# Kernel optimization log

Hardware: AMD Instinct MI355X
Metric: run time of the kernel (lower is better)

## Reference

```python
import jax, jax.numpy as jnp
import numpy as np

DIM = 128
EDGE_COUNT = 128
N_NODES = 128
GRAPH_COUNT = 8
VOCAB = 100000
VEC_DIM = 300


def setup_inputs():
    key = jax.random.key(0)
    ks = jax.random.split(key, 8)
    rng = np.random.default_rng(0)
    data = jnp.asarray(rng.integers(0, VOCAB, size=N_NODES), dtype=jnp.int32)
    types = jnp.zeros((N_NODES,), dtype=jnp.int32)  # single data_type
    edges = jnp.asarray(rng.integers(0, EDGE_COUNT, size=N_NODES), dtype=jnp.int32)
    # parent-offset trees: node i's parent is a node > i, last node is the single root (offset 0)
    g = np.zeros((GRAPH_COUNT, N_NODES), dtype=np.int32)
    for j in range(GRAPH_COUNT):
        for i in range(N_NODES - 1):
            p = int(rng.integers(i + 1, N_NODES))
            g[j, i] = p - i
    graphs = jnp.asarray(g)
    inv_sqrt_d = 1.0 / np.sqrt(DIM)
    inv_sqrt_v = 1.0 / np.sqrt(VEC_DIM)
    return {
        "data": data, "types": types, "graphs": graphs, "edges": edges, "pos": 37,
        "data_vecs": jax.random.normal(ks[0], (VOCAB, VEC_DIM), jnp.float32),
        "data_weights": jax.random.normal(ks[1], (VEC_DIM, DIM), jnp.float32) * inv_sqrt_v,
        "data_biases": jax.random.normal(ks[2], (DIM,), jnp.float32) * 0.1,
        "edge_weights": jax.random.normal(ks[3], (EDGE_COUNT, DIM, DIM), jnp.float32) * inv_sqrt_d,
        "edge_biases": jax.random.normal(ks[4], (EDGE_COUNT, DIM), jnp.float32) * 0.1,
        "score_embedding_weights": jax.random.normal(ks[5], (DIM, 1), jnp.float32) * inv_sqrt_d,
        "score_data_weights": jax.random.normal(ks[6], (DIM, 1), jnp.float32) * inv_sqrt_d,
        "score_bias": jax.random.normal(ks[7], (1, 1), jnp.float32),
    }


def _tree_structure(parents_row):
    # Faithful reproduction of calc_embedding's structure handling (numpy on int constants).
    parents = np.asarray(parents_row).copy()
    n = len(parents)
    roots = [i for i in range(n) if parents[i] == 0]
    for i in range(len(roots) - 1):
        parents[roots[i]] = roots[i + 1]
    root = roots[-1]
    parents[root] = -n
    children = {}
    for i in range(n):
        pp = i + int(parents[i])
        children.setdefault(pp, []).append(i)
    order = []  # DFS preorder from root; reversed gives children-before-parent
    stack = [root]
    while stack:
        node = stack.pop()
        order.append(node)
        stack.extend(children.get(node, []))
    return root, children, order


def _forward(data, types, graphs, edges, pos,
             data_vecs, data_weights, data_biases,
             edge_weights, edge_biases,
             score_embedding_weights, score_data_weights, score_bias):
    data_np = np.asarray(data)
    graphs_np = np.asarray(graphs)
    edges_np = np.asarray(edges).copy()
    E, D, _ = edge_weights.shape
    # data embedding + data score for the queried position
    d_emb = data_vecs[data_np[pos]] @ data_weights + data_biases          # (D,)
    d_score = score_bias[0, 0] + d_emb @ score_data_weights[:, 0]         # scalar
    edges_np[pos] = -1  # unknown edge at pos -> branch over all edge types
    # base embeddings for all nodes at once: (N, D)
    base = data_vecs[data_np] @ data_weights + data_biases

    def transform(child_emb, eid):
        # child_emb: (E, D). eid < 0 -> per-edge-type weights (baddbmm over all E edges)
        if eid < 0:
            return jnp.einsum('ed,edk->ek', child_emb, edge_weights) + edge_biases
        return child_emb @ edge_weights[eid] + edge_biases[eid]

    scores = []
    for j in range(graphs_np.shape[0]):
        root, children, order = _tree_structure(graphs_np[j])
        emb = {}
        for n in reversed(order):  # children before parents
            e = jnp.broadcast_to(base[n], (E, D))
            ch = children.get(n, [])
            for c in ch:
                e = e + transform(emb.pop(c), int(edges_np[c]))
            if ch:
                e = jax.nn.relu(e)  # clamp(min=0) only for internal nodes
            emb[n] = e
        res = transform(emb[root], int(edges_np[root]))  # add_child_embedding(zeros, root_emb, edges[root])
        scores.append(d_score + res @ score_embedding_weights[:, 0])  # (E,)
    return jnp.stack(scores)  # (GRAPH_COUNT, EDGE_COUNT)


def reference(data, types, graphs, edges, pos, data_vecs, data_weights, data_biases,
              edge_weights, edge_biases, score_embedding_weights, score_data_weights, score_bias):
    return _forward(data, types, graphs, edges, pos, data_vecs, data_weights, data_biases,
                    edge_weights, edge_biases, score_embedding_weights, score_data_weights, score_bias)
```

## Files before the change

kernel.cpp:

```cpp
#include <hip/hip_runtime.h>
#include <stdint.h>


#define NND 128
#define DD  128
#define GG  8
#define VD  300
#define EDGEN 128
#define CH2 16

typedef unsigned int u32;

#define F_POS  (1<<16)
#define F_PATH (1<<17)

__global__ void __launch_bounds__(128) k_base(
        const int* __restrict__ data, const int* __restrict__ posArr,
        const float* __restrict__ vecs, const float* __restrict__ dw,
        const float* __restrict__ db,   const float* __restrict__ sdw,
        const float* __restrict__ sb,
        float* __restrict__ base, float* __restrict__ dscore)
{
    __shared__ __align__(16) float row[VD];
    __shared__ float red[DD];
    int n = blockIdx.x, t = threadIdx.x;
    int id = data[n];
    const float4* vp = (const float4*)(vecs + (size_t)id * VD);
    for (int i = t; i < VD/4; i += 128) ((float4*)row)[i] = vp[i];
    __syncthreads();
    float a0 = db[t], a1 = 0.f, a2 = 0.f, a3 = 0.f;
    for (int d = 0; d < VD; d += 4){
        a0 = fmaf(row[d+0], dw[(d+0)*DD + t], a0);
        a1 = fmaf(row[d+1], dw[(d+1)*DD + t], a1);
        a2 = fmaf(row[d+2], dw[(d+2)*DD + t], a2);
        a3 = fmaf(row[d+3], dw[(d+3)*DD + t], a3);
    }
    float acc = (a0 + a1) + (a2 + a3);
    base[n*DD + t] = acc;
    if (n == posArr[0]){
        red[t] = acc * sdw[t];
        __syncthreads();
        for (int o = 64; o > 0; o >>= 1){ if (t < o) red[t] += red[t+o]; __syncthreads(); }
        if (t == 0) dscore[0] = sb[0] + red[0];
    }
}

__global__ void __launch_bounds__(1024, 1) k_tree(
        const int* __restrict__ graphs, const int* __restrict__ edges,
        const int* __restrict__ posArr, const float* __restrict__ EW,
        const float* __restrict__ EB,   const float* __restrict__ base,
        float* __restrict__ vposG, float* __restrict__ uG, int* __restrict__ meta)
{
    __shared__ __align__(16) float contrib[NND-1][DD];
    __shared__ int par_s[NND], eid_s[NND], flg_s[NND];
    __shared__ int ccnt[NND], cstart[NND], cidx[NND];
    __shared__ int dep[NND], anc[NND], lcnt[NND], lstart[NND], order[NND];
    __shared__ int maxD_s;

    int g = blockIdx.x, t = threadIdx.x;

    if (t < NND){
        par_s[t] = (t < NND-1) ? (t + graphs[g*NND + t]) : (NND-1);
        eid_s[t] = edges[t];
        flg_s[t] = 0;
        ccnt[t]  = 0;
        lcnt[t]  = 0;
    }
    if (t == 0) maxD_s = 0;
    __syncthreads();

    int mySlot = 0;
    if (t < NND-1){
        int p = par_s[t];
        atomicAdd(&ccnt[p], 1);
        for (int c = 0; c < t; ++c) mySlot += (par_s[c] == p);
    }
    if (t < NND){
        dep[t] = (t < NND-1) ? 1 : 0;
        anc[t] = par_s[t];
    }
    if (t == 0){
        int p = posArr[0];
        flg_s[p] |= F_POS;
        int c = par_s[p], s = 0;
        for (;;){
            flg_s[c] |= F_PATH | (s << 24);
            meta[g*(NND+1) + 1 + s] = c;
            ++s;
            if (c == NND-1) break;
            c = par_s[c];
        }
        meta[g*(NND+1)] = s;
    }
    __syncthreads();

    if (t < NND){
        int s = 0;
        for (int p = 0; p < t; ++p) s += ccnt[p];
        cstart[t] = s;
    }
    __syncthreads();
    if (t < NND-1) cidx[cstart[par_s[t]] + mySlot] = t;

    for (int k = 0; k < 7; ++k){
        int d2 = 0, a2 = 0;
        if (t < NND){ d2 = dep[t] + dep[anc[t]]; a2 = anc[anc[t]]; }
        __syncthreads();
        if (t < NND){ dep[t] = d2; anc[t] = a2; }
        __syncthreads();
    }
    if (t < NND) atomicMax(&maxD_s, dep[t]);
    if (t < NND) atomicAdd(&lcnt[dep[t]], 1);
    __syncthreads();

    if (t < NND){
        int s = 0;
        for (int d2 = 0; d2 < t; ++d2) s += lcnt[d2];
        lstart[t] = s;
    }
    __syncthreads();
    if (t < NND){
        int d2 = dep[t], s = 0;
        for (int c = 0; c < t; ++c) s += (dep[c] == d2);
        order[lstart[d2] + s] = t;
    }
    __syncthreads();

    int w = t >> 6, l = t & 63;
    int c0 = 2*l;
    int li = l & 31, hl = l >> 5;
    int c4 = 4*li, dbase = 64*hl;
    int maxD = maxD_s;

    for (int d = maxD; d >= 0; --d){
        int lo = lstart[d], cnt = lcnt[d];
        for (int q = w; q < cnt; q += 16){
            int n = order[lo + q];
            float2 bse = *(const float2*)&base[n*DD + c0];
            float e0 = bse.x, e1 = bse.y;
            int cs = cstart[n], cc = ccnt[n];
            for (int j = 0; j < cc; ++j){
                int c = cidx[cs + j];
                if (!(flg_s[c] & (F_POS | F_PATH))){
                    float2 cv = *(const float2*)&contrib[c][c0];
                    e0 += cv.x; e1 += cv.y;
                }
            }
            int f = flg_s[n];
            if (f & F_POS){
                if (cc){ e0 = fmaxf(e0, 0.f); e1 = fmaxf(e1, 0.f); }
                *(float2*)&vposG[g*DD + c0] = make_float2(e0, e1);
            } else if (f & F_PATH){
                int slot = ((u32)f) >> 24;
                *(float2*)&uG[((size_t)g*NND + slot)*DD + c0] = make_float2(e0, e1);
            } else {
                if (cc){ e0 = fmaxf(e0, 0.f); e1 = fmaxf(e1, 0.f); }
                *(float2*)&contrib[n][c0] = make_float2(e0, e1);
                asm volatile("s_waitcnt lgkmcnt(0)" ::: "memory");
                int e = eid_s[n];
                const float* Wp = EW + (size_t)e*(DD*DD) + (size_t)dbase*DD + c4;
                const float* xr = &contrib[n][dbase];
                float4 A[8], B[8];
                float s0=0.f, s1=0.f, s2=0.f, s3=0.f;
                #define LW(buf, gi) { _Pragma("unroll") \
                    for (int j2 = 0; j2 < 8; ++j2) \
                        buf[j2] = *(const float4*)&Wp[(size_t)((gi)*8 + j2)*DD]; }
                #define CP(buf, gi) { _Pragma("unroll") \
                    for (int j2 = 0; j2 < 8; ++j2){ \
                        float x = xr[(gi)*8 + j2]; \
                        s0 = fmaf(x, buf[j2].x, s0); s1 = fmaf(x, buf[j2].y, s1); \
                        s2 = fmaf(x, buf[j2].z, s2); s3 = fmaf(x, buf[j2].w, s3); } }
                LW(A,0); LW(B,1);
                CP(A,0); LW(A,2);
                CP(B,1); LW(B,3);
                CP(A,2); LW(A,4);
                CP(B,3); LW(B,5);
                CP(A,4); LW(A,6);
                CP(B,5); LW(B,7);
                CP(A,6);
                CP(B,7);
                #undef LW
                #undef CP
                s0 += __shfl_xor(s0, 32);
                s1 += __shfl_xor(s1, 32);
                s2 += __shfl_xor(s2, 32);
                s3 += __shfl_xor(s3, 32);
                if (hl == 0){
                    float4 bb = *(const float4*)&EB[(size_t)e*DD + c4];
                    *(float4*)&contrib[n][c4] =
                        make_float4(s0 + bb.x, s1 + bb.y, s2 + bb.z, s3 + bb.w);
                }
            }
        }
        __syncthreads();
    }
}

__global__ void __launch_bounds__(256, 1) k_step0(
        const float* __restrict__ EW, const float* __restrict__ EB,
        const float* __restrict__ vposG, const float* __restrict__ uG,
        float* __restrict__ V0)
{
    __shared__ __align__(16) float vpos_s[GG][DD];
    int e = blockIdx.x, t = threadIdx.x, l = t & 63, w = t >> 6;
    {
        int idx = t;
        ((float4*)vpos_s)[idx] = ((const float4*)vposG)[idx];
    }
    __syncthreads();
    int k4 = w*8 + (l & 7);
    int d0 = (l >> 3) * 16;
    bool owner = ((l >> 3) == 0);
    const float* Wp = EW + (size_t)e*(DD*DD) + (size_t)d0*DD + 4*k4;
    float4 wr[16];
    #pragma unroll
    for (int d = 0; d < 16; ++d) wr[d] = *(const float4*)&Wp[d*DD];
    float4 bb = *(const float4*)&EB[(size_t)e*DD + 4*k4];
    for (int g = 0; g < GG; ++g){
        float s0=0.f, s1=0.f, s2=0.f, s3=0.f;
        #pragma unroll
        for (int d = 0; d < 16; ++d){
            float x = vpos_s[g][d0 + d];
            s0 = fmaf(x, wr[d].x, s0);
            s1 = fmaf(x, wr[d].y, s1);
            s2 = fmaf(x, wr[d].z, s2);
            s3 = fmaf(x, wr[d].w, s3);
        }
        #pragma unroll
        for (int m = 8; m <= 32; m <<= 1){
            s0 += __shfl_xor(s0, m); s1 += __shfl_xor(s1, m);
            s2 += __shfl_xor(s2, m); s3 += __shfl_xor(s3, m);
        }
        if (owner){
            float4 u0 = *(const float4*)&uG[(size_t)g*NND*DD + 4*k4];
            float4 r;
            r.x = fmaxf(u0.x + s0 + bb.x, 0.f);
            r.y = fmaxf(u0.y + s1 + bb.y, 0.f);
            r.z = fmaxf(u0.z + s2 + bb.z, 0.f);
            r.w = fmaxf(u0.w + s3 + bb.w, 0.f);
            *(float4*)&V0[((size_t)g*EDGEN + e)*DD + 4*k4] = r;
        }
    }
}

__global__ void __launch_bounds__(256, 1) k_steps(
        const int* __restrict__ edges,
        const float* __restrict__ EW, const float* __restrict__ EB,
        const float* __restrict__ SEW,
        const float* __restrict__ uG, const float* __restrict__ V0,
        const int* __restrict__ meta, const float* __restrict__ dscore,
        float* __restrict__ outp)
{
    __shared__ __align__(16) float Vbuf[2][CH2][DD];
    __shared__ float red[CH2][4];
    int g = blockIdx.x >> 3, chunk = blockIdx.x & 7;
    int t = threadIdx.x, l = t & 63, w = t >> 6;
    int k4 = w*8 + (l & 7);
    int d0 = (l >> 3) * 16;
    bool owner = ((l >> 3) == 0);
    int eBase = chunk * CH2;
    int L = meta[g*(NND+1)];

    for (int idx = t; idx < CH2*DD/4; idx += 256)
        ((float4*)&Vbuf[0][0][0])[idx] =
            ((const float4*)&V0[((size_t)g*EDGEN + eBase)*DD])[idx];
    __syncthreads();

    int cur = 0;
    for (int s = 1; s < L; ++s){
        int pn = meta[g*(NND+1) + s];
        int ej = edges[pn];
        const float* Wp = EW + (size_t)ej*(DD*DD) + (size_t)d0*DD + 4*k4;
        float4 wr[16];
        #pragma unroll
        for (int d = 0; d < 16; ++d) wr[d] = *(const float4*)&Wp[d*DD];
        float4 us = *(const float4*)&uG[((size_t)g*NND + s)*DD + 4*k4];
        float4 bb = *(const float4*)&EB[(size_t)ej*DD + 4*k4];
        #pragma unroll 4
        for (int p = 0; p < CH2; ++p){
            float ev[16];
            #pragma unroll
            for (int j = 0; j < 4; ++j){
                float4 x = *(const float4*)&Vbuf[cur][p][d0 + 4*j];
                ev[4*j+0]=x.x; ev[4*j+1]=x.y; ev[4*j+2]=x.z; ev[4*j+3]=x.w;
            }
            float s0=0.f, s1=0.f, s2=0.f, s3=0.f;
            #pragma unroll
            for (int d = 0; d < 16; ++d){
                s0 = fmaf(ev[d], wr[d].x, s0);
                s1 = fmaf(ev[d], wr[d].y, s1);
                s2 = fmaf(ev[d], wr[d].z, s2);
                s3 = fmaf(ev[d], wr[d].w, s3);
            }
            #pragma unroll
            for (int m = 8; m <= 32; m <<= 1){
                s0 += __shfl_xor(s0, m); s1 += __shfl_xor(s1, m);
                s2 += __shfl_xor(s2, m); s3 += __shfl_xor(s3, m);
            }
            if (owner){
                float4 r;
                r.x = fmaxf(us.x + s0 + bb.x, 0.f);
                r.y = fmaxf(us.y + s1 + bb.y, 0.f);
                r.z = fmaxf(us.z + s2 + bb.z, 0.f);
                r.w = fmaxf(us.w + s3 + bb.w, 0.f);
                *(float4*)&Vbuf[cur^1][p][4*k4] = r;
            }
        }
        __syncthreads();
        cur ^= 1;
    }

    {
        int rn = meta[g*(NND+1) + L];
        int er = edges[rn];
        const float* Wp = EW + (size_t)er*(DD*DD) + (size_t)d0*DD + 4*k4;
        float4 wr[16];
        #pragma unroll
        for (int d = 0; d < 16; ++d) wr[d] = *(const float4*)&Wp[d*DD];
        float4 bb = *(const float4*)&EB[(size_t)er*DD + 4*k4];
        float4 sw = *(const float4*)&SEW[4*k4];
        #pragma unroll 4
        for (int p = 0; p < CH2; ++p){
            float ev[16];
            #pragma unroll
            for (int j = 0; j < 4; ++j){
                float4 x = *(const float4*)&Vbuf[cur][p][d0 + 4*j];
                ev[4*j+0]=x.x; ev[4*j+1]=x.y; ev[4*j+2]=x.z; ev[4*j+3]=x.w;
            }
            float s0=0.f, s1=0.f, s2=0.f, s3=0.f;
            #pragma unroll
            for (int d = 0; d < 16; ++d){
                s0 = fmaf(ev[d], wr[d].x, s0);
                s1 = fmaf(ev[d], wr[d].y, s1);
                s2 = fmaf(ev[d], wr[d].z, s2);
                s3 = fmaf(ev[d], wr[d].w, s3);
            }
            #pragma unroll
            for (int m = 8; m <= 32; m <<= 1){
                s0 += __shfl_xor(s0, m); s1 += __shfl_xor(s1, m);
                s2 += __shfl_xor(s2, m); s3 += __shfl_xor(s3, m);
            }
            if (owner){
                float part = (s0 + bb.x) * sw.x + (s1 + bb.y) * sw.y
                           + (s2 + bb.z) * sw.z + (s3 + bb.w) * sw.w;
                part += __shfl_xor(part, 1);
                part += __shfl_xor(part, 2);
                part += __shfl_xor(part, 4);
                if (l == 0) red[p][w] = part;
            }
        }
        __syncthreads();
        if (t < CH2)
            outp[g*DD + eBase + t] = dscore[0] + red[t][0] + red[t][1] + red[t][2] + red[t][3];
    }
}

extern "C" void kernel_launch(void* const* d_in, const int* in_sizes, int n_in,
                              void* d_out, int out_size, void* d_ws, size_t ws_size,
                              hipStream_t stream)
{
    const int*   data   = (const int*)d_in[0];
    const int*   graphs = (const int*)d_in[2];
    const int*   edges  = (const int*)d_in[3];
    const int*   posArr = (const int*)d_in[4];
    const float* vecs   = (const float*)d_in[5];
    const float* dw     = (const float*)d_in[6];
    const float* db     = (const float*)d_in[7];
    const float* ew     = (const float*)d_in[8];
    const float* eb     = (const float*)d_in[9];
    const float* sew    = (const float*)d_in[10];
    const float* sdw    = (const float*)d_in[11];
    const float* sb     = (const float*)d_in[12];

    char* ws = (char*)d_ws;
    float* base   = (float*)(ws);
    float* vposG  = (float*)(ws + 65536);
    float* uG     = (float*)(ws + 65536 + 4096);
    float* dscore = (float*)(ws + 593920);
    int*   meta   = (int*)  (ws + 594176);
    float* V0     = (float*)(ws + 598528);

    float* outp = (float*)d_out;

    k_base <<<NND, 128, 0, stream>>>(data, posArr, vecs, dw, db, sdw, sb, base, dscore);
    k_tree <<<GG, 1024, 0, stream>>>(graphs, edges, posArr, ew, eb, base, vposG, uG, meta);
    k_step0<<<EDGEN, 256, 0, stream>>>(ew, eb, vposG, uG, V0);
    k_steps<<<GG*(EDGEN/CH2), 256, 0, stream>>>(edges, ew, eb, sew, uG, V0, meta, dscore, outp);
}
```

Measured before the change: 345.8 us.

## Fuse base embedding and step0 into tree and chain kernels, pair tree GEMVs

The base-embedding kernel is folded into the tree kernel, so each tree block recomputes all node base rows in shared-memory tiles. The first chain step is folded into the chain kernel, so V0 is computed in place instead of going through a global round trip and a separate launch. Inside the tree level loop each wave now handles two nodes at once and interleaves their weight loads, to get more memory-level parallelism on a latency-bound dependency chain. In exchange, the base GEMV work is repeated in every graph block and the step0 weights are re-read per graph chunk.

```diff
diff --git a/kernel.cpp b/kernel.cpp
--- a/kernel.cpp
+++ b/kernel.cpp
@@ -14,41 +14,14 @@
 #define F_POS  (1<<16)
 #define F_PATH (1<<17)
 
-__global__ void __launch_bounds__(128) k_base(
-        const int* __restrict__ data, const int* __restrict__ posArr,
+__global__ void __launch_bounds__(1024, 1) k_tree2(
+        const int* __restrict__ data,   const int* __restrict__ graphs,
+        const int* __restrict__ edges,  const int* __restrict__ posArr,
         const float* __restrict__ vecs, const float* __restrict__ dw,
         const float* __restrict__ db,   const float* __restrict__ sdw,
         const float* __restrict__ sb,
-        float* __restrict__ base, float* __restrict__ dscore)
-{
-    __shared__ __align__(16) float row[VD];
-    __shared__ float red[DD];
-    int n = blockIdx.x, t = threadIdx.x;
-    int id = data[n];
-    const float4* vp = (const float4*)(vecs + (size_t)id * VD);
-    for (int i = t; i < VD/4; i += 128) ((float4*)row)[i] = vp[i];
-    __syncthreads();
-    float a0 = db[t], a1 = 0.f, a2 = 0.f, a3 = 0.f;
-    for (int d = 0; d < VD; d += 4){
-        a0 = fmaf(row[d+0], dw[(d+0)*DD + t], a0);
-        a1 = fmaf(row[d+1], dw[(d+1)*DD + t], a1);
-        a2 = fmaf(row[d+2], dw[(d+2)*DD + t], a2);
-        a3 = fmaf(row[d+3], dw[(d+3)*DD + t], a3);
-    }
-    float acc = (a0 + a1) + (a2 + a3);
-    base[n*DD + t] = acc;
-    if (n == posArr[0]){
-        red[t] = acc * sdw[t];
-        __syncthreads();
-        for (int o = 64; o > 0; o >>= 1){ if (t < o) red[t] += red[t+o]; __syncthreads(); }
-        if (t == 0) dscore[0] = sb[0] + red[0];
-    }
-}
-
-__global__ void __launch_bounds__(1024, 1) k_tree(
-        const int* __restrict__ graphs, const int* __restrict__ edges,
-        const int* __restrict__ posArr, const float* __restrict__ EW,
-        const float* __restrict__ EB,   const float* __restrict__ base,
+        const float* __restrict__ EW,   const float* __restrict__ EB,
+        float* __restrict__ base, float* __restrict__ dscore,
         float* __restrict__ vposG, float* __restrict__ uG, int* __restrict__ meta)
 {
     __shared__ __align__(16) float contrib[NND-1][DD];
@@ -58,6 +31,38 @@
     __shared__ int maxD_s;
 
     int g = blockIdx.x, t = threadIdx.x;
+
+    {
+        float* rowbuf = &contrib[0][0];
+        for (int tile = 0; tile < 16; ++tile){
+            for (int i = t; i < 8*75; i += 1024){
+                int r = i / 75, el = i - r*75;
+                int nn = tile*8 + r;
+                ((float4*)&rowbuf[r*304])[el] =
+                    ((const float4*)&vecs[(size_t)data[nn]*VD])[el];
+            }
+            __syncthreads();
+            int r = t >> 7, c = t & 127;
+            int nn = tile*8 + r;
+            const float* rb = &rowbuf[r*304];
+            float a0 = db[c], a1 = 0.f, a2 = 0.f, a3 = 0.f;
+            for (int d = 0; d < VD; d += 4){
+                a0 = fmaf(rb[d+0], dw[(d+0)*DD + c], a0);
+                a1 = fmaf(rb[d+1], dw[(d+1)*DD + c], a1);
+                a2 = fmaf(rb[d+2], dw[(d+2)*DD + c], a2);
+                a3 = fmaf(rb[d+3], dw[(d+3)*DD + c], a3);
+            }
+            base[nn*DD + c] = (a0 + a1) + (a2 + a3);
+            __syncthreads();
+        }
+        int p = posArr[0];
+        float* red = rowbuf;
+        if (t < DD) red[t] = base[p*DD + t] * sdw[t];
+        __syncthreads();
+        for (int o = 64; o > 0; o >>= 1){ if (t < o) red[t] += red[t+o]; __syncthreads(); }
+        if (t == 0) dscore[0] = sb[0] + red[0];
+        __syncthreads();
+    }
 
     if (t < NND){
         par_s[t] = (t < NND-1) ? (t + graphs[g*NND + t]) : (NND-1);
@@ -132,122 +137,147 @@
     int c4 = 4*li, dbase = 64*hl;
     int maxD = maxD_s;
 
+    auto prep = [&](int n)->bool{
+        float2 bse = *(const float2*)&base[n*DD + c0];
+        float e0 = bse.x, e1 = bse.y;
+        int cs = cstart[n], cc = ccnt[n];
+        for (int j = 0; j < cc; ++j){
+            int c = cidx[cs + j];
+            if (!(flg_s[c] & (F_POS | F_PATH))){
+                float2 cv = *(const float2*)&contrib[c][c0];
+                e0 += cv.x; e1 += cv.y;
+            }
+        }
+        int f = flg_s[n];
+        if (f & F_POS){
+            if (cc){ e0 = fmaxf(e0, 0.f); e1 = fmaxf(e1, 0.f); }
+            *(float2*)&vposG[g*DD + c0] = make_float2(e0, e1);
+            return false;
+        }
+        if (f & F_PATH){
+            int slot = ((u32)f) >> 24;
+            *(float2*)&uG[((size_t)g*NND + slot)*DD + c0] = make_float2(e0, e1);
+            return false;
+        }
+        if (cc){ e0 = fmaxf(e0, 0.f); e1 = fmaxf(e1, 0.f); }
+        *(float2*)&contrib[n][c0] = make_float2(e0, e1);
+        return true;
+    };
+
+    auto gemv1 = [&](int n){
+        int e = eid_s[n];
+        const float* Wp = EW + (size_t)e*(DD*DD) + (size_t)dbase*DD + c4;
+        const float* xr = &contrib[n][dbase];
+        float4 A[8], B[8];
+        float s0=0.f, s1=0.f, s2=0.f, s3=0.f;
+        #define LW(buf, gi) { _Pragma("unroll") \
+            for (int j2 = 0; j2 < 8; ++j2) \
+                buf[j2] = *(const float4*)&Wp[(size_t)((gi)*8 + j2)*DD]; }
+        #define CP(buf, gi) { _Pragma("unroll") \
+            for (int j2 = 0; j2 < 8; ++j2){ \
+                float x = xr[(gi)*8 + j2]; \
+                s0 = fmaf(x, buf[j2].x, s0); s1 = fmaf(x, buf[j2].y, s1); \
+                s2 = fmaf(x, buf[j2].z, s2); s3 = fmaf(x, buf[j2].w, s3); } }
+        LW(A,0); LW(B,1);
+        CP(A,0); LW(A,2);
+        CP(B,1); LW(B,3);
+        CP(A,2); LW(A,4);
+        CP(B,3); LW(B,5);
+        CP(A,4); LW(A,6);
+        CP(B,5); LW(B,7);
+        CP(A,6);
+        CP(B,7);
+        #undef LW
+        #undef CP
+        s0 += __shfl_xor(s0, 32); s1 += __shfl_xor(s1, 32);
+        s2 += __shfl_xor(s2, 32); s3 += __shfl_xor(s3, 32);
+        if (hl == 0){
+            float4 bb = *(const float4*)&EB[(size_t)e*DD + c4];
+            *(float4*)&contrib[n][c4] =
+                make_float4(s0 + bb.x, s1 + bb.y, s2 + bb.z, s3 + bb.w);
+        }
+    };
+
+    auto gemv2 = [&](int n1, int n2){
+        int ea = eid_s[n1], eb = eid_s[n2];
+        const float* W1 = EW + (size_t)ea*(DD*DD) + (size_t)dbase*DD + c4;
+        const float* W2 = EW + (size_t)eb*(DD*DD) + (size_t)dbase*DD + c4;
+        const float* x1 = &contrib[n1][dbase];
+        const float* x2 = &contrib[n2][dbase];
+        float4 A[8], B[8];
+        float a0=0.f,a1=0.f,a2=0.f,a3=0.f, b0=0.f,b1=0.f,b2=0.f,b3=0.f;
+        #define LW1(gi) { _Pragma("unroll") \
+            for (int j2 = 0; j2 < 8; ++j2) \
+                A[j2] = *(const float4*)&W1[(size_t)((gi)*8 + j2)*DD]; }
+        #define LW2(gi) { _Pragma("unroll") \
+            for (int j2 = 0; j2 < 8; ++j2) \
+                B[j2] = *(const float4*)&W2[(size_t)((gi)*8 + j2)*DD]; }
+        #define CP1(gi) { _Pragma("unroll") \
+            for (int j2 = 0; j2 < 8; ++j2){ \
+                float x = x1[(gi)*8 + j2]; \
+                a0 = fmaf(x, A[j2].x, a0); a1 = fmaf(x, A[j2].y, a1); \
+                a2 = fmaf(x, A[j2].z, a2); a3 = fmaf(x, A[j2].w, a3); } }
+        #define CP2(gi) { _Pragma("unroll") \
+            for (int j2 = 0; j2 < 8; ++j2){ \
+                float x = x2[(gi)*8 + j2]; \
+                b0 = fmaf(x, B[j2].x, b0); b1 = fmaf(x, B[j2].y, b1); \
+                b2 = fmaf(x, B[j2].z, b2); b3 = fmaf(x, B[j2].w, b3); } }
+        LW1(0); LW2(0);
+        CP1(0); LW1(1);
+        CP2(0); LW2(1);
+        CP1(1); LW1(2);
+        CP2(1); LW2(2);
+        CP1(2); LW1(3);
+        CP2(2); LW2(3);
+        CP1(3); LW1(4);
+        CP2(3); LW2(4);
+        CP1(4); LW1(5);
+        CP2(4); LW2(5);
+        CP1(5); LW1(6);
+        CP2(5); LW2(6);
+        CP1(6); LW1(7);
+        CP2(6); LW2(7);
+        CP1(7);
+        CP2(7);
+        #undef LW1
+        #undef LW2
+        #undef CP1
+        #undef CP2
+        a0 += __shfl_xor(a0, 32); a1 += __shfl_xor(a1, 32);
+        a2 += __shfl_xor(a2, 32); a3 += __shfl_xor(a3, 32);
+        b0 += __shfl_xor(b0, 32); b1 += __shfl_xor(b1, 32);
+        b2 += __shfl_xor(b2, 32); b3 += __shfl_xor(b3, 32);
+        if (hl == 0){
+            float4 ba = *(const float4*)&EB[(size_t)ea*DD + c4];
+            float4 bb = *(const float4*)&EB[(size_t)eb*DD + c4];
+            *(float4*)&contrib[n1][c4] =
+                make_float4(a0 + ba.x, a1 + ba.y, a2 + ba.z, a3 + ba.w);
+            *(float4*)&contrib[n2][c4] =
+                make_float4(b0 + bb.x, b1 + bb.y, b2 + bb.z, b3 + bb.w);
+        }
+    };
+
     for (int d = maxD; d >= 0; --d){
         int lo = lstart[d], cnt = lcnt[d];
-        for (int q = w; q < cnt; q += 16){
-            int n = order[lo + q];
-            float2 bse = *(const float2*)&base[n*DD + c0];
-            float e0 = bse.x, e1 = bse.y;
-            int cs = cstart[n], cc = ccnt[n];
-            for (int j = 0; j < cc; ++j){
-                int c = cidx[cs + j];
-                if (!(flg_s[c] & (F_POS | F_PATH))){
-                    float2 cv = *(const float2*)&contrib[c][c0];
-                    e0 += cv.x; e1 += cv.y;
-                }
-            }
-            int f = flg_s[n];
-            if (f & F_POS){
-                if (cc){ e0 = fmaxf(e0, 0.f); e1 = fmaxf(e1, 0.f); }
-                *(float2*)&vposG[g*DD + c0] = make_float2(e0, e1);
-            } else if (f & F_PATH){
-                int slot = ((u32)f) >> 24;
-                *(float2*)&uG[((size_t)g*NND + slot)*DD + c0] = make_float2(e0, e1);
-            } else {
-                if (cc){ e0 = fmaxf(e0, 0.f); e1 = fmaxf(e1, 0.f); }
-                *(float2*)&contrib[n][c0] = make_float2(e0, e1);
-                asm volatile("s_waitcnt lgkmcnt(0)" ::: "memory");
-                int e = eid_s[n];
-                const float* Wp = EW + (size_t)e*(DD*DD) + (size_t)dbase*DD + c4;
-                const float* xr = &contrib[n][dbase];
-                float4 A[8], B[8];
-                float s0=0.f, s1=0.f, s2=0.f, s3=0.f;
-                #define LW(buf, gi) { _Pragma("unroll") \
-                    for (int j2 = 0; j2 < 8; ++j2) \
-                        buf[j2] = *(const float4*)&Wp[(size_t)((gi)*8 + j2)*DD]; }
-                #define CP(buf, gi) { _Pragma("unroll") \
-                    for (int j2 = 0; j2 < 8; ++j2){ \
-                        float x = xr[(gi)*8 + j2]; \
-                        s0 = fmaf(x, buf[j2].x, s0); s1 = fmaf(x, buf[j2].y, s1); \
-                        s2 = fmaf(x, buf[j2].z, s2); s3 = fmaf(x, buf[j2].w, s3); } }
-                LW(A,0); LW(B,1);
-                CP(A,0); LW(A,2);
-                CP(B,1); LW(B,3);
-                CP(A,2); LW(A,4);
-                CP(B,3); LW(B,5);
-                CP(A,4); LW(A,6);
-                CP(B,5); LW(B,7);
-                CP(A,6);
-                CP(B,7);
-                #undef LW
-                #undef CP
-                s0 += __shfl_xor(s0, 32);
-                s1 += __shfl_xor(s1, 32);
-                s2 += __shfl_xor(s2, 32);
-                s3 += __shfl_xor(s3, 32);
-                if (hl == 0){
-                    float4 bb = *(const float4*)&EB[(size_t)e*DD + c4];
-                    *(float4*)&contrib[n][c4] =
-                        make_float4(s0 + bb.x, s1 + bb.y, s2 + bb.z, s3 + bb.w);
-                }
-            }
+        for (int q = w; q < cnt; q += 32){
+            int n1 = order[lo + q];
+            int n2 = (q + 16 < cnt) ? order[lo + q + 16] : -1;
+            bool p1 = prep(n1);
+            bool p2 = (n2 >= 0) ? prep(n2) : false;
+            asm volatile("s_waitcnt lgkmcnt(0)" ::: "memory");
+            if (p1 && p2)      gemv2(n1, n2);
+            else { if (p1) gemv1(n1);
+                   if (p2) gemv1(n2); }
         }
         __syncthreads();
     }
 }
 
-__global__ void __launch_bounds__(256, 1) k_step0(
-        const float* __restrict__ EW, const float* __restrict__ EB,
-        const float* __restrict__ vposG, const float* __restrict__ uG,
-        float* __restrict__ V0)
-{
-    __shared__ __align__(16) float vpos_s[GG][DD];
-    int e = blockIdx.x, t = threadIdx.x, l = t & 63, w = t >> 6;
-    {
-        int idx = t;
-        ((float4*)vpos_s)[idx] = ((const float4*)vposG)[idx];
-    }
-    __syncthreads();
-    int k4 = w*8 + (l & 7);
-    int d0 = (l >> 3) * 16;
-    bool owner = ((l >> 3) == 0);
-    const float* Wp = EW + (size_t)e*(DD*DD) + (size_t)d0*DD + 4*k4;
-    float4 wr[16];
-    #pragma unroll
-    for (int d = 0; d < 16; ++d) wr[d] = *(const float4*)&Wp[d*DD];
-    float4 bb = *(const float4*)&EB[(size_t)e*DD + 4*k4];
-    for (int g = 0; g < GG; ++g){
-        float s0=0.f, s1=0.f, s2=0.f, s3=0.f;
-        #pragma unroll
-        for (int d = 0; d < 16; ++d){
-            float x = vpos_s[g][d0 + d];
-            s0 = fmaf(x, wr[d].x, s0);
-            s1 = fmaf(x, wr[d].y, s1);
-            s2 = fmaf(x, wr[d].z, s2);
-            s3 = fmaf(x, wr[d].w, s3);
-        }
-        #pragma unroll
-        for (int m = 8; m <= 32; m <<= 1){
-            s0 += __shfl_xor(s0, m); s1 += __shfl_xor(s1, m);
-            s2 += __shfl_xor(s2, m); s3 += __shfl_xor(s3, m);
-        }
-        if (owner){
-            float4 u0 = *(const float4*)&uG[(size_t)g*NND*DD + 4*k4];
-            float4 r;
-            r.x = fmaxf(u0.x + s0 + bb.x, 0.f);
-            r.y = fmaxf(u0.y + s1 + bb.y, 0.f);
-            r.z = fmaxf(u0.z + s2 + bb.z, 0.f);
-            r.w = fmaxf(u0.w + s3 + bb.w, 0.f);
-            *(float4*)&V0[((size_t)g*EDGEN + e)*DD + 4*k4] = r;
-        }
-    }
-}
-
-__global__ void __launch_bounds__(256, 1) k_steps(
+__global__ void __launch_bounds__(256, 1) k_chain2(
         const int* __restrict__ edges,
         const float* __restrict__ EW, const float* __restrict__ EB,
         const float* __restrict__ SEW,
-        const float* __restrict__ uG, const float* __restrict__ V0,
+        const float* __restrict__ vposG, const float* __restrict__ uG,
         const int* __restrict__ meta, const float* __restrict__ dscore,
         float* __restrict__ outp)
 {
@@ -261,9 +291,42 @@
     int eBase = chunk * CH2;
     int L = meta[g*(NND+1)];
 
-    for (int idx = t; idx < CH2*DD/4; idx += 256)
-        ((float4*)&Vbuf[0][0][0])[idx] =
-            ((const float4*)&V0[((size_t)g*EDGEN + eBase)*DD])[idx];
+    float vpf[16];
+    #pragma unroll
+    for (int j = 0; j < 4; ++j){
+        float4 x = *(const float4*)&vposG[g*DD + d0 + 4*j];
+        vpf[4*j+0]=x.x; vpf[4*j+1]=x.y; vpf[4*j+2]=x.z; vpf[4*j+3]=x.w;
+    }
+    float4 u0 = *(const float4*)&uG[(size_t)g*NND*DD + 4*k4];
+
+    #pragma unroll 2
+    for (int p = 0; p < CH2; ++p){
+        int e = eBase + p;
+        const float* Wp = EW + (size_t)e*(DD*DD) + (size_t)d0*DD + 4*k4;
+        float s0=0.f, s1=0.f, s2=0.f, s3=0.f;
+        #pragma unroll
+        for (int d = 0; d < 16; ++d){
+            float4 wv = *(const float4*)&Wp[d*DD];
+            s0 = fmaf(vpf[d], wv.x, s0);
+            s1 = fmaf(vpf[d], wv.y, s1);
+            s2 = fmaf(vpf[d], wv.z, s2);
+            s3 = fmaf(vpf[d], wv.w, s3);
+        }
+        #pragma unroll
+        for (int m = 8; m <= 32; m <<= 1){
+            s0 += __shfl_xor(s0, m); s1 += __shfl_xor(s1, m);
+            s2 += __shfl_xor(s2, m); s3 += __shfl_xor(s3, m);
+        }
+        if (owner){
+            float4 bb = *(const float4*)&EB[(size_t)e*DD + 4*k4];
+            float4 r;
+            r.x = fmaxf(u0.x + s0 + bb.x, 0.f);
+            r.y = fmaxf(u0.y + s1 + bb.y, 0.f);
+            r.z = fmaxf(u0.z + s2 + bb.z, 0.f);
+            r.w = fmaxf(u0.w + s3 + bb.w, 0.f);
+            *(float4*)&Vbuf[0][p][4*k4] = r;
+        }
+    }
     __syncthreads();
 
     int cur = 0;
@@ -375,15 +438,14 @@
     char* ws = (char*)d_ws;
     float* base   = (float*)(ws);
     float* vposG  = (float*)(ws + 65536);
-    float* uG     = (float*)(ws + 65536 + 4096);
+    float* uG     = (float*)(ws + 69632);
     float* dscore = (float*)(ws + 593920);
     int*   meta   = (int*)  (ws + 594176);
-    float* V0     = (float*)(ws + 598528);
 
     float* outp = (float*)d_out;
 
-    k_base <<<NND, 128, 0, stream>>>(data, posArr, vecs, dw, db, sdw, sb, base, dscore);
-    k_tree <<<GG, 1024, 0, stream>>>(graphs, edges, posArr, ew, eb, base, vposG, uG, meta);
-    k_step0<<<EDGEN, 256, 0, stream>>>(ew, eb, vposG, uG, V0);
-    k_steps<<<GG*(EDGEN/CH2), 256, 0, stream>>>(edges, ew, eb, sew, uG, V0, meta, dscore, outp);
+    k_tree2 <<<GG, 1024, 0, stream>>>(data, graphs, edges, posArr, vecs, dw, db,
+                                      sdw, sb, ew, eb, base, dscore, vposG, uG, meta);
+    k_chain2<<<GG*(EDGEN/CH2), 256, 0, stream>>>(edges, ew, eb, sew, vposG, uG,
+                                                 meta, dscore, outp);
 }
```

Measured after the change: 526.4 us. +52.2%, slower.

## Replace level-synchronous tree traversal with dataflow work queue in k_tree

Applied to the files above, without the earlier changes.

Drops the pointer-jumping depth computation and the per-level __syncthreads loop in the tree kernel. Each wavefront now pulls ready nodes from a shared-memory queue, and a node's parent is enqueued once its child counter reaches zero. This removes block-wide barriers and load imbalance across depth levels, so independent subtrees can proceed concurrently. The cost is spin-waiting on queue slots and atomics, plus reliance on volatile LDS polling and waitcnt for correct ordering.

```diff
diff --git a/kernel.cpp b/kernel.cpp
--- a/kernel.cpp
+++ b/kernel.cpp
@@ -54,8 +54,9 @@
     __shared__ __align__(16) float contrib[NND-1][DD];
     __shared__ int par_s[NND], eid_s[NND], flg_s[NND];
     __shared__ int ccnt[NND], cstart[NND], cidx[NND];
-    __shared__ int dep[NND], anc[NND], lcnt[NND], lstart[NND], order[NND];
-    __shared__ int maxD_s;
+    __shared__ int kcnt[NND];
+    __shared__ int queue[NND];
+    __shared__ int qhead, qtail;
 
     int g = blockIdx.x, t = threadIdx.x;
 
@@ -64,9 +65,9 @@
         eid_s[t] = edges[t];
         flg_s[t] = 0;
         ccnt[t]  = 0;
-        lcnt[t]  = 0;
-    }
-    if (t == 0) maxD_s = 0;
+        queue[t] = -1;
+    }
+    if (t == 0){ qhead = 0; qtail = 0; }
     __syncthreads();
 
     int mySlot = 0;
@@ -74,10 +75,6 @@
         int p = par_s[t];
         atomicAdd(&ccnt[p], 1);
         for (int c = 0; c < t; ++c) mySlot += (par_s[c] == p);
-    }
-    if (t < NND){
-        dep[t] = (t < NND-1) ? 1 : 0;
-        anc[t] = par_s[t];
     }
     if (t == 0){
         int p = posArr[0];
@@ -98,101 +95,102 @@
         int s = 0;
         for (int p = 0; p < t; ++p) s += ccnt[p];
         cstart[t] = s;
+        kcnt[t] = ccnt[t];
     }
     __syncthreads();
     if (t < NND-1) cidx[cstart[par_s[t]] + mySlot] = t;
-
-    for (int k = 0; k < 7; ++k){
-        int d2 = 0, a2 = 0;
-        if (t < NND){ d2 = dep[t] + dep[anc[t]]; a2 = anc[anc[t]]; }
-        __syncthreads();
-        if (t < NND){ dep[t] = d2; anc[t] = a2; }
-        __syncthreads();
-    }
-    if (t < NND) atomicMax(&maxD_s, dep[t]);
-    if (t < NND) atomicAdd(&lcnt[dep[t]], 1);
-    __syncthreads();
-
-    if (t < NND){
-        int s = 0;
-        for (int d2 = 0; d2 < t; ++d2) s += lcnt[d2];
-        lstart[t] = s;
-    }
-    __syncthreads();
-    if (t < NND){
-        int d2 = dep[t], s = 0;
-        for (int c = 0; c < t; ++c) s += (dep[c] == d2);
-        order[lstart[d2] + s] = t;
-    }
-    __syncthreads();
-
-    int w = t >> 6, l = t & 63;
+    if (t < NND && ccnt[t] == 0){
+        int slot = atomicAdd(&qtail, 1);
+        queue[slot] = t;
+    }
+    __syncthreads();
+
+    int l = t & 63;
     int c0 = 2*l;
     int li = l & 31, hl = l >> 5;
     int c4 = 4*li, dbase = 64*hl;
-    int maxD = maxD_s;
-
-    for (int d = maxD; d >= 0; --d){
-        int lo = lstart[d], cnt = lcnt[d];
-        for (int q = w; q < cnt; q += 16){
-            int n = order[lo + q];
-            float2 bse = *(const float2*)&base[n*DD + c0];
-            float e0 = bse.x, e1 = bse.y;
-            int cs = cstart[n], cc = ccnt[n];
-            for (int j = 0; j < cc; ++j){
-                int c = cidx[cs + j];
-                if (!(flg_s[c] & (F_POS | F_PATH))){
-                    float2 cv = *(const float2*)&contrib[c][c0];
-                    e0 += cv.x; e1 += cv.y;
-                }
-            }
-            int f = flg_s[n];
-            if (f & F_POS){
-                if (cc){ e0 = fmaxf(e0, 0.f); e1 = fmaxf(e1, 0.f); }
-                *(float2*)&vposG[g*DD + c0] = make_float2(e0, e1);
-            } else if (f & F_PATH){
-                int slot = ((u32)f) >> 24;
-                *(float2*)&uG[((size_t)g*NND + slot)*DD + c0] = make_float2(e0, e1);
-            } else {
-                if (cc){ e0 = fmaxf(e0, 0.f); e1 = fmaxf(e1, 0.f); }
-                *(float2*)&contrib[n][c0] = make_float2(e0, e1);
-                asm volatile("s_waitcnt lgkmcnt(0)" ::: "memory");
-                int e = eid_s[n];
-                const float* Wp = EW + (size_t)e*(DD*DD) + (size_t)dbase*DD + c4;
-                const float* xr = &contrib[n][dbase];
-                float4 A[8], B[8];
-                float s0=0.f, s1=0.f, s2=0.f, s3=0.f;
-                #define LW(buf, gi) { _Pragma("unroll") \
-                    for (int j2 = 0; j2 < 8; ++j2) \
-                        buf[j2] = *(const float4*)&Wp[(size_t)((gi)*8 + j2)*DD]; }
-                #define CP(buf, gi) { _Pragma("unroll") \
-                    for (int j2 = 0; j2 < 8; ++j2){ \
-                        float x = xr[(gi)*8 + j2]; \
-                        s0 = fmaf(x, buf[j2].x, s0); s1 = fmaf(x, buf[j2].y, s1); \
-                        s2 = fmaf(x, buf[j2].z, s2); s3 = fmaf(x, buf[j2].w, s3); } }
-                LW(A,0); LW(B,1);
-                CP(A,0); LW(A,2);
-                CP(B,1); LW(B,3);
-                CP(A,2); LW(A,4);
-                CP(B,3); LW(B,5);
-                CP(A,4); LW(A,6);
-                CP(B,5); LW(B,7);
-                CP(A,6);
-                CP(B,7);
-                #undef LW
-                #undef CP
-                s0 += __shfl_xor(s0, 32);
-                s1 += __shfl_xor(s1, 32);
-                s2 += __shfl_xor(s2, 32);
-                s3 += __shfl_xor(s3, 32);
-                if (hl == 0){
-                    float4 bb = *(const float4*)&EB[(size_t)e*DD + c4];
-                    *(float4*)&contrib[n][c4] =
-                        make_float4(s0 + bb.x, s1 + bb.y, s2 + bb.z, s3 + bb.w);
-                }
-            }
-        }
-        __syncthreads();
+
+    auto prep = [&](int n)->bool{
+        float2 bse = *(const float2*)&base[n*DD + c0];
+        float e0 = bse.x, e1 = bse.y;
+        int cs = cstart[n], cc = ccnt[n];
+        for (int j = 0; j < cc; ++j){
+            int c = cidx[cs + j];
+            if (!(flg_s[c] & (F_POS | F_PATH))){
+                float2 cv = *(const float2*)&contrib[c][c0];
+                e0 += cv.x; e1 += cv.y;
+            }
+        }
+        int f = flg_s[n];
+        if (f & F_POS){
+            if (cc){ e0 = fmaxf(e0, 0.f); e1 = fmaxf(e1, 0.f); }
+            *(float2*)&vposG[g*DD + c0] = make_float2(e0, e1);
+            return false;
+        }
+        if (f & F_PATH){
+            int slot = ((u32)f) >> 24;
+            *(float2*)&uG[((size_t)g*NND + slot)*DD + c0] = make_float2(e0, e1);
+            return false;
+        }
+        if (cc){ e0 = fmaxf(e0, 0.f); e1 = fmaxf(e1, 0.f); }
+        *(float2*)&contrib[n][c0] = make_float2(e0, e1);
+        return true;
+    };
+
+    auto gemv1 = [&](int n){
+        int e = eid_s[n];
+        const float* Wp = EW + (size_t)e*(DD*DD) + (size_t)dbase*DD + c4;
+        const float* xr = &contrib[n][dbase];
+        float4 A[8], B[8];
+        float s0=0.f, s1=0.f, s2=0.f, s3=0.f;
+        #define LW(buf, gi) { _Pragma("unroll") \
+            for (int j2 = 0; j2 < 8; ++j2) \
+                buf[j2] = *(const float4*)&Wp[(size_t)((gi)*8 + j2)*DD]; }
+        #define CP(buf, gi) { _Pragma("unroll") \
+            for (int j2 = 0; j2 < 8; ++j2){ \
+                float x = xr[(gi)*8 + j2]; \
+                s0 = fmaf(x, buf[j2].x, s0); s1 = fmaf(x, buf[j2].y, s1); \
+                s2 = fmaf(x, buf[j2].z, s2); s3 = fmaf(x, buf[j2].w, s3); } }
+        LW(A,0); LW(B,1);
+        CP(A,0); LW(A,2);
+        CP(B,1); LW(B,3);
+        CP(A,2); LW(A,4);
+        CP(B,3); LW(B,5);
+        CP(A,4); LW(A,6);
+        CP(B,5); LW(B,7);
+        CP(A,6);
+        CP(B,7);
+        #undef LW
+        #undef CP
+        s0 += __shfl_xor(s0, 32); s1 += __shfl_xor(s1, 32);
+        s2 += __shfl_xor(s2, 32); s3 += __shfl_xor(s3, 32);
+        if (hl == 0){
+            float4 bb = *(const float4*)&EB[(size_t)e*DD + c4];
+            *(float4*)&contrib[n][c4] =
+                make_float4(s0 + bb.x, s1 + bb.y, s2 + bb.z, s3 + bb.w);
+        }
+    };
+
+    for (;;){
+        int idx = 0;
+        if (l == 0) idx = atomicAdd(&qhead, 1);
+        idx = __shfl(idx, 0);
+        if (idx >= NND) break;
+        volatile int* qp = (volatile int*)&queue[idx];
+        int n;
+        while ((n = *qp) < 0) ;
+        bool doG = prep(n);
+        asm volatile("s_waitcnt lgkmcnt(0)" ::: "memory");
+        if (doG) gemv1(n);
+        asm volatile("s_waitcnt lgkmcnt(0)" ::: "memory");
+        if (l == 0 && n != NND-1){
+            int p = par_s[n];
+            int old = atomicSub(&kcnt[p], 1);
+            if (old == 1){
+                int slot = atomicAdd(&qtail, 1);
+                queue[slot] = p;
+            }
+        }
     }
 }
 
@@ -375,7 +373,7 @@
     char* ws = (char*)d_ws;
     float* base   = (float*)(ws);
     float* vposG  = (float*)(ws + 65536);
-    float* uG     = (float*)(ws + 65536 + 4096);
+    float* uG     = (float*)(ws + 69632);
     float* dscore = (float*)(ws + 593920);
     int*   meta   = (int*)  (ws + 594176);
     float* V0     = (float*)(ws + 598528);
@@ -385,5 +383,6 @@
     k_base <<<NND, 128, 0, stream>>>(data, posArr, vecs, dw, db, sdw, sb, base, dscore);
     k_tree <<<GG, 1024, 0, stream>>>(graphs, edges, posArr, ew, eb, base, vposG, uG, meta);
     k_step0<<<EDGEN, 256, 0, stream>>>(ew, eb, vposG, uG, V0);
-    k_steps<<<GG*(EDGEN/CH2), 256, 0, stream>>>(edges, ew, eb, sew, uG, V0, meta, dscore, outp);
-}
+    k_steps<<<GG*(EDGEN/CH2), 256, 0, stream>>>(edges, ew, eb, sew, uG, V0,
+                                                meta, dscore, outp);
+}
```

New measurement: 341.2 us. Within noise of the previous version (-1.3%).

## Split each tree across eight cooperating blocks with global per-level barriers

Applied to the files above, without the earlier changes.

The tree kernel now runs eight blocks per graph instead of one. Nodes within each depth level are interleaved across those blocks, and child contributions are exchanged through a global buffer that aliases V0 rather than living in shared memory. Blocks synchronise after each level with an atomic counter and spin-wait, and the counters are zeroed in k_base. The aim is to spread the edge-weight matvec streaming over more compute units. In exchange it adds global-memory traffic and per-level barrier latency, and it relies on all 64 blocks being resident at once.

```diff
diff --git a/kernel.cpp b/kernel.cpp
--- a/kernel.cpp
+++ b/kernel.cpp
@@ -8,22 +8,26 @@
 #define VD  300
 #define EDGEN 128
 #define CH2 16
+#define KSP 8
 
 typedef unsigned int u32;
 
 #define F_POS  (1<<16)
 #define F_PATH (1<<17)
+#define SKIPF  (F_POS|F_PATH)
 
 __global__ void __launch_bounds__(128) k_base(
         const int* __restrict__ data, const int* __restrict__ posArr,
         const float* __restrict__ vecs, const float* __restrict__ dw,
         const float* __restrict__ db,   const float* __restrict__ sdw,
         const float* __restrict__ sb,
-        float* __restrict__ base, float* __restrict__ dscore)
+        float* __restrict__ base, float* __restrict__ dscore,
+        int* __restrict__ flagsG)
 {
     __shared__ __align__(16) float row[VD];
     __shared__ float red[DD];
     int n = blockIdx.x, t = threadIdx.x;
+    if (n < GG) flagsG[n*NND + t] = 0;
     int id = data[n];
     const float4* vp = (const float4*)(vecs + (size_t)id * VD);
     for (int i = t; i < VD/4; i += 128) ((float4*)row)[i] = vp[i];
@@ -45,19 +49,20 @@
     }
 }
 
-__global__ void __launch_bounds__(1024, 1) k_tree(
+__global__ void __launch_bounds__(1024, 1) k_treeX(
         const int* __restrict__ graphs, const int* __restrict__ edges,
         const int* __restrict__ posArr, const float* __restrict__ EW,
         const float* __restrict__ EB,   const float* __restrict__ base,
-        float* __restrict__ vposG, float* __restrict__ uG, int* __restrict__ meta)
+        float* __restrict__ vposG, float* __restrict__ uG, int* __restrict__ meta,
+        float* __restrict__ contribX, int* __restrict__ flagsG)
 {
-    __shared__ __align__(16) float contrib[NND-1][DD];
+    __shared__ __align__(16) float xstage[16][DD];
     __shared__ int par_s[NND], eid_s[NND], flg_s[NND];
     __shared__ int ccnt[NND], cstart[NND], cidx[NND];
     __shared__ int dep[NND], anc[NND], lcnt[NND], lstart[NND], order[NND];
     __shared__ int maxD_s;
 
-    int g = blockIdx.x, t = threadIdx.x;
+    int b = blockIdx.x, g = b >> 3, k = b & (KSP-1), t = threadIdx.x;
 
     if (t < NND){
         par_s[t] = (t < NND-1) ? (t + graphs[g*NND + t]) : (NND-1);
@@ -85,12 +90,12 @@
         int c = par_s[p], s = 0;
         for (;;){
             flg_s[c] |= F_PATH | (s << 24);
-            meta[g*(NND+1) + 1 + s] = c;
+            if (k == 0) meta[g*(NND+1) + 1 + s] = c;
             ++s;
             if (c == NND-1) break;
             c = par_s[c];
         }
-        meta[g*(NND+1)] = s;
+        if (k == 0) meta[g*(NND+1)] = s;
     }
     __syncthreads();
 
@@ -102,7 +107,7 @@
     __syncthreads();
     if (t < NND-1) cidx[cstart[par_s[t]] + mySlot] = t;
 
-    for (int k = 0; k < 7; ++k){
+    for (int kk = 0; kk < 7; ++kk){
         int d2 = 0, a2 = 0;
         if (t < NND){ d2 = dep[t] + dep[anc[t]]; a2 = anc[anc[t]]; }
         __syncthreads();
@@ -134,17 +139,26 @@
 
     for (int d = maxD; d >= 0; --d){
         int lo = lstart[d], cnt = lcnt[d];
-        for (int q = w; q < cnt; q += 16){
+        for (int q = k + KSP*w; q < cnt; q += KSP*16){
             int n = order[lo + q];
             float2 bse = *(const float2*)&base[n*DD + c0];
             float e0 = bse.x, e1 = bse.y;
             int cs = cstart[n], cc = ccnt[n];
-            for (int j = 0; j < cc; ++j){
-                int c = cidx[cs + j];
-                if (!(flg_s[c] & (F_POS | F_PATH))){
-                    float2 cv = *(const float2*)&contrib[c][c0];
-                    e0 += cv.x; e1 += cv.y;
-                }
+            for (int j0 = 0; j0 < cc; j0 += 4){
+                float2 v0, v1, v2, v3;
+                int u0=0, u1=0, u2=0, u3=0;
+                if (j0+0 < cc){ int c = cidx[cs+j0+0];
+                    if (!(flg_s[c] & SKIPF)){ v0 = *(const float2*)&contribX[((size_t)g*NND+c)*DD + c0]; u0=1; } }
+                if (j0+1 < cc){ int c = cidx[cs+j0+1];
+                    if (!(flg_s[c] & SKIPF)){ v1 = *(const float2*)&contribX[((size_t)g*NND+c)*DD + c0]; u1=1; } }
+                if (j0+2 < cc){ int c = cidx[cs+j0+2];
+                    if (!(flg_s[c] & SKIPF)){ v2 = *(const float2*)&contribX[((size_t)g*NND+c)*DD + c0]; u2=1; } }
+                if (j0+3 < cc){ int c = cidx[cs+j0+3];
+                    if (!(flg_s[c] & SKIPF)){ v3 = *(const float2*)&contribX[((size_t)g*NND+c)*DD + c0]; u3=1; } }
+                if (u0){ e0 += v0.x; e1 += v0.y; }
+                if (u1){ e0 += v1.x; e1 += v1.y; }
+                if (u2){ e0 += v2.x; e1 += v2.y; }
+                if (u3){ e0 += v3.x; e1 += v3.y; }
             }
             int f = flg_s[n];
             if (f & F_POS){
@@ -155,11 +169,11 @@
                 *(float2*)&uG[((size_t)g*NND + slot)*DD + c0] = make_float2(e0, e1);
             } else {
                 if (cc){ e0 = fmaxf(e0, 0.f); e1 = fmaxf(e1, 0.f); }
-                *(float2*)&contrib[n][c0] = make_float2(e0, e1);
+                *(float2*)&xstage[w][c0] = make_float2(e0, e1);
                 asm volatile("s_waitcnt lgkmcnt(0)" ::: "memory");
                 int e = eid_s[n];
                 const float* Wp = EW + (size_t)e*(DD*DD) + (size_t)dbase*DD + c4;
-                const float* xr = &contrib[n][dbase];
+                const float* xr = &xstage[w][dbase];
                 float4 A[8], B[8];
                 float s0=0.f, s1=0.f, s2=0.f, s3=0.f;
                 #define LW(buf, gi) { _Pragma("unroll") \
@@ -181,18 +195,27 @@
                 CP(B,7);
                 #undef LW
                 #undef CP
-                s0 += __shfl_xor(s0, 32);
-                s1 += __shfl_xor(s1, 32);
-                s2 += __shfl_xor(s2, 32);
-                s3 += __shfl_xor(s3, 32);
+                s0 += __shfl_xor(s0, 32); s1 += __shfl_xor(s1, 32);
+                s2 += __shfl_xor(s2, 32); s3 += __shfl_xor(s3, 32);
                 if (hl == 0){
                     float4 bb = *(const float4*)&EB[(size_t)e*DD + c4];
-                    *(float4*)&contrib[n][c4] =
+                    *(float4*)&contribX[((size_t)g*NND + n)*DD + c4] =
                         make_float4(s0 + bb.x, s1 + bb.y, s2 + bb.z, s3 + bb.w);
                 }
             }
         }
         __syncthreads();
+        if (d > 0){
+            if (t == 0){
+                __threadfence();
+                atomicAdd(&flagsG[g*NND + d], 1);
+                while (__hip_atomic_load(&flagsG[g*NND + d],
+                        __ATOMIC_ACQUIRE, __HIP_MEMORY_SCOPE_AGENT) < KSP)
+                    __builtin_amdgcn_s_sleep(1);
+                __threadfence();
+            }
+            __syncthreads();
+        }
     }
 }
 
@@ -375,15 +398,20 @@
     char* ws = (char*)d_ws;
     float* base   = (float*)(ws);
     float* vposG  = (float*)(ws + 65536);
-    float* uG     = (float*)(ws + 65536 + 4096);
+    float* uG     = (float*)(ws + 69632);
     float* dscore = (float*)(ws + 593920);
     int*   meta   = (int*)  (ws + 594176);
     float* V0     = (float*)(ws + 598528);
+    float* contribX = V0;
+    int*   flagsG = (int*)  (ws + 1122816);
 
     float* outp = (float*)d_out;
 
-    k_base <<<NND, 128, 0, stream>>>(data, posArr, vecs, dw, db, sdw, sb, base, dscore);
-    k_tree <<<GG, 1024, 0, stream>>>(graphs, edges, posArr, ew, eb, base, vposG, uG, meta);
+    k_base <<<NND, 128, 0, stream>>>(data, posArr, vecs, dw, db, sdw, sb,
+                                     base, dscore, flagsG);
+    k_treeX<<<GG*KSP, 1024, 0, stream>>>(graphs, edges, posArr, ew, eb, base,
+                                         vposG, uG, meta, contribX, flagsG);
     k_step0<<<EDGEN, 256, 0, stream>>>(ew, eb, vposG, uG, V0);
-    k_steps<<<GG*(EDGEN/CH2), 256, 0, stream>>>(edges, ew, eb, sew, uG, V0, meta, dscore, outp);
+    k_steps<<<GG*(EDGEN/CH2), 256, 0, stream>>>(edges, ew, eb, sew, uG, V0,
+                                                meta, dscore, outp);
 }
```

New measurement: 318.5 us. 1.09x faster.
